# Performance work log

Measured on AMD Instinct MI355X. Metric: run time of the kernel, lower is better.

## Reference

```python
import jax, jax.numpy as jnp
import numpy as np

N, E, EE = 2048, 32768, 262144
CS, CZ, CG, NRBF = 384, 128, 16, 64
D_MIN, D_MAX = 0.0, 20.0
LN_EPS = 1e-5
EPS = 1e-8


def _p(key, shape, scale):
    return (jax.random.normal(key, shape, dtype=jnp.float32) * scale)


def setup_inputs() -> dict:
    key = jax.random.key(0)
    ks = jax.random.split(key, 40)
    inp = {
        "node_features": jax.random.normal(ks[0], (N, CS), dtype=jnp.float32),
        "node_trans": jax.random.normal(ks[1], (N, 3), dtype=jnp.float32) * 5.0,
        "dst_edge_features": jax.random.normal(ks[2], (E, CZ), dtype=jnp.float32),
        "dst_edge_index": jax.random.randint(ks[3], (2, E), 0, N),
        "src_edge_features": jax.random.normal(ks[4], (E, CZ), dtype=jnp.float32),
        "src_edge_index": jax.random.randint(ks[5], (2, E), 0, N),
        "edge_edge_index": jax.random.randint(ks[6], (2, EE), 0, E),
        # params (torch Linear math: y = x @ W + b, W stored [in,out])
        "w_nl": _p(ks[7], (CS, CG), 0.05), "b_nl": jnp.zeros((CG,), jnp.float32),
        "w_nr": _p(ks[8], (CS, CG), 0.05), "b_nr": jnp.zeros((CG,), jnp.float32),
        "g_dst": jnp.ones((CZ,), jnp.float32), "bt_dst": jnp.zeros((CZ,), jnp.float32),
        "g_src": jnp.ones((CZ,), jnp.float32), "bt_src": jnp.zeros((CZ,), jnp.float32),
        "w_ep": _p(ks[9], (CZ, CZ), 0.08), "b_ep": jnp.zeros((CZ,), jnp.float32),
        "w_eg": _p(ks[10], (CZ, CZ), 0.08), "b_eg": jnp.zeros((CZ,), jnp.float32),
        "w_dg": _p(ks[11], (CG * CG, CZ), 0.06), "b_dg": jnp.zeros((CZ,), jnp.float32),
        "w_dp": _p(ks[12], (NRBF, CZ), 0.1), "b_dp": jnp.zeros((CZ,), jnp.float32),
        "g_out": jnp.ones((CZ,), jnp.float32), "bt_out": jnp.zeros((CZ,), jnp.float32),
        "w_lo": _p(ks[13], (CZ, CZ), 0.08), "b_lo": jnp.zeros((CZ,), jnp.float32),
        "w_og": _p(ks[14], (CZ, CZ), 0.08), "b_og": jnp.zeros((CZ,), jnp.float32),
    }
    return inp


def _ln(x, g, b):
    m = jnp.mean(x, axis=-1, keepdims=True)
    v = jnp.mean(jnp.square(x - m), axis=-1, keepdims=True)
    return (x - m) * jax.lax.rsqrt(v + LN_EPS) * g + b


def _rbf(d):
    mu = jnp.linspace(D_MIN, D_MAX, NRBF)  # [NRBF]
    sigma = (D_MAX - D_MIN) / NRBF
    return jnp.exp(-jnp.square((d[:, None] - mu) / sigma))  # [EE, NRBF]


def reference(node_features, node_trans, dst_edge_features, dst_edge_index,
              src_edge_features, src_edge_index, edge_edge_index,
              w_nl, b_nl, w_nr, b_nr, g_dst, bt_dst, g_src, bt_src,
              w_ep, b_ep, w_eg, b_eg, w_dg, b_dg, w_dp, b_dp,
              g_out, bt_out, w_lo, b_lo, w_og, b_og):
    ee0 = edge_edge_index[0]  # index into dst edges
    ee1 = edge_edge_index[1]  # index into src edges
    n1 = src_edge_index[0][ee1]  # left node per edge-edge pair
    n2 = dst_edge_index[0][ee0]  # right node per edge-edge pair

    dst_ef = _ln(dst_edge_features, g_dst, bt_dst)
    src_ef = _ln(src_edge_features, g_src, bt_src)

    node_left = node_features @ w_nl + b_nl   # [N, CG]
    node_right = node_features @ w_nr + b_nr  # [N, CG]

    # per-pair outer product gate: [EE, CG*CG]
    edge3 = jnp.einsum('ei,ej->eij', node_left[n1], node_right[n2]).reshape(-1, CG * CG)
    edge3_gate = edge3 @ w_dg + b_dg  # [EE, CZ]

    diff = node_trans[n1] - node_trans[n2] + EPS
    dist = jnp.linalg.norm(diff, axis=-1)  # [EE]
    dist_feat = _rbf(dist) @ w_dp + b_dp   # [EE, CZ]
    edge3_features = jax.nn.sigmoid(edge3_gate) * dist_feat

    edge2 = jax.nn.sigmoid(src_ef @ w_eg + b_eg) * (src_ef @ w_ep + b_ep)  # [E, CZ]
    edge_update = edge2[ee0] * edge3_features  # [EE, CZ]
    edge_update = jax.ops.segment_sum(edge_update, ee0, num_segments=E)  # [E, CZ]

    edge_update = _ln(edge_update, g_out, bt_out)
    edge_update = edge_update @ w_lo + b_lo
    edge_update = edge_update * jax.nn.sigmoid(dst_ef @ w_og + b_og)
    return edge_update
```

## Files before the change

kernel.cpp:

```cpp
#include <hip/hip_runtime.h>
#include <hip/hip_bf16.h>
#include <math.h>

#define NN    2048
#define NE    32768
#define NP    262144
#define CS_   384
#define CZ_   128
#define CG_   16
#define NRBF_ 64

typedef __attribute__((ext_vector_type(8))) short bf16x8;
typedef __attribute__((ext_vector_type(4))) float f32x4;

__device__ __forceinline__ unsigned short f2bf(float f) {
  __hip_bfloat16 h = __float2bfloat16(f);
  union { __hip_bfloat16 h; unsigned short u; } cv; cv.h = h; return cv.u;
}

__global__ void k_nodeproj(const float* __restrict__ nf,
                           const float* __restrict__ wnl, const float* __restrict__ bnl,
                           const float* __restrict__ wnr, const float* __restrict__ bnr,
                           unsigned short* __restrict__ nl, unsigned short* __restrict__ nr) {
  const int n = blockIdx.x;
  const int t = threadIdx.x;
  if (t >= 32) return;
  const float* __restrict__ w = (t < 16) ? wnl : wnr;
  const int col = t & 15;
  const float* __restrict__ row = nf + (size_t)n * CS_;
  float acc = 0.f;
  #pragma unroll 8
  for (int k = 0; k < CS_; ++k) acc = fmaf(row[k], w[k * CG_ + col], acc);
  acc += (t < 16) ? bnl[col] : bnr[col];
  ((t < 16) ? nl : nr)[n * CG_ + col] = f2bf(acc);
}

__global__ void k_prepB(const float* __restrict__ wdg, const float* __restrict__ wdp,
                        unsigned short* __restrict__ frag) {
  const int idx = blockIdx.x * 256 + threadIdx.x;
  if (idx >= 40960) return;
  float v;
  if (idx < 32768) {
    const int e = idx & 7, l = (idx >> 3) & 63, ks = (idx >> 9) & 7, n = idx >> 12;
    const int k = ks * 32 + (l >> 4) * 8 + e, ch = n * 16 + (l & 15);
    v = wdg[(size_t)k * CZ_ + ch];
  } else {
    const int j = idx - 32768;
    const int e = j & 7, l = (j >> 3) & 63, ks2 = (j >> 9) & 1, n = j >> 10;
    const int k2 = ks2 * 32 + (l >> 4) * 8 + e, ch = n * 16 + (l & 15);
    v = wdp[(size_t)k2 * CZ_ + ch];
  }
  frag[idx] = f2bf(v);
}

__global__ void k_hist(const int* __restrict__ ee, int* __restrict__ hist) {
  const int p = blockIdx.x * 256 + threadIdx.x;
  atomicAdd(&hist[ee[p]], 1);
}

__global__ __launch_bounds__(1024) void k_scan(const int* __restrict__ hist,
                                               int* __restrict__ start) {
  __shared__ int tot[1024];
  const int t = threadIdx.x;
  const int base = t * 32;
  int s = 0;
  for (int k = 0; k < 32; ++k) s += hist[base + k];
  tot[t] = s;
  __syncthreads();
  for (int off = 1; off < 1024; off <<= 1) {
    int v = tot[t];
    int u = (t >= off) ? tot[t - off] : 0;
    __syncthreads();
    tot[t] = v + u;
    __syncthreads();
  }
  int run = (t == 0) ? 0 : tot[t - 1];
  for (int k = 0; k < 32; ++k) { start[base + k] = run; run += hist[base + k]; }
  if (t == 1023) start[32768] = run;
}

__global__ void k_scatter(const int* __restrict__ ee, const int* __restrict__ start,
                          int* __restrict__ cnt2, int* __restrict__ perm) {
  const int p = blockIdx.x * 256 + threadIdx.x;
  const int e = ee[p];
  const int idx = atomicAdd(&cnt2[e], 1);
  perm[start[e] + idx] = p;
}

__global__ __launch_bounds__(256) void k_edge2(
    const float* __restrict__ sef,
    const float* __restrict__ gs, const float* __restrict__ bs,
    const float* __restrict__ weg, const float* __restrict__ beg,
    const float* __restrict__ wep, const float* __restrict__ bep,
    float* __restrict__ edge2) {
  __shared__ float xln[32][132];
  const int tid = threadIdx.x;
  const int row0 = blockIdx.x * 32;
  {
    const int r = tid >> 3, s = tid & 7;
    const float* __restrict__ xp = sef + (size_t)(row0 + r) * CZ_ + s * 16;
    float v[16];
    #pragma unroll
    for (int q = 0; q < 4; ++q) {
      const float4 t4 = *(const float4*)(xp + 4 * q);
      v[4*q+0] = t4.x; v[4*q+1] = t4.y; v[4*q+2] = t4.z; v[4*q+3] = t4.w;
    }
    float sum = 0.f, sq = 0.f;
    #pragma unroll
    for (int q = 0; q < 16; ++q) { sum += v[q]; sq = fmaf(v[q], v[q], sq); }
    #pragma unroll
    for (int o = 1; o < 8; o <<= 1) { sum += __shfl_xor(sum, o); sq += __shfl_xor(sq, o); }
    const float mean = sum * (1.f / CZ_);
    const float rstd = rsqrtf(sq * (1.f / CZ_) - mean * mean + 1e-5f);
    const int kb = s * 16;
    #pragma unroll
    for (int q = 0; q < 16; ++q)
      xln[r][kb + q] = (v[q] - mean) * rstd * gs[kb + q] + bs[kb + q];
  }
  __syncthreads();

  const int c = tid & (CZ_ - 1);
  const int h = tid >> 7;
  float accg[16], accp[16];
  #pragma unroll
  for (int q = 0; q < 16; ++q) { accg[q] = 0.f; accp[q] = 0.f; }
  #pragma unroll 2
  for (int k = 0; k < CZ_; k += 4) {
    const float wg0 = weg[(size_t)(k+0)*CZ_ + c], wg1 = weg[(size_t)(k+1)*CZ_ + c],
                wg2 = weg[(size_t)(k+2)*CZ_ + c], wg3 = weg[(size_t)(k+3)*CZ_ + c];
    const float wp0 = wep[(size_t)(k+0)*CZ_ + c], wp1 = wep[(size_t)(k+1)*CZ_ + c],
                wp2 = wep[(size_t)(k+2)*CZ_ + c], wp3 = wep[(size_t)(k+3)*CZ_ + c];
    #pragma unroll
    for (int rr = 0; rr < 16; ++rr) {
      const float4 xv = *(const float4*)&xln[h*16 + rr][k];
      accg[rr] = fmaf(xv.x, wg0, accg[rr]); accg[rr] = fmaf(xv.y, wg1, accg[rr]);
      accg[rr] = fmaf(xv.z, wg2, accg[rr]); accg[rr] = fmaf(xv.w, wg3, accg[rr]);
      accp[rr] = fmaf(xv.x, wp0, accp[rr]); accp[rr] = fmaf(xv.y, wp1, accp[rr]);
      accp[rr] = fmaf(xv.z, wp2, accp[rr]); accp[rr] = fmaf(xv.w, wp3, accp[rr]);
    }
  }
  const float bg = beg[c], bp = bep[c];
  #pragma unroll
  for (int rr = 0; rr < 16; ++rr) {
    const float gate = 1.f / (1.f + __expf(-(accg[rr] + bg)));
    edge2[(size_t)(row0 + h*16 + rr) * CZ_ + c] = gate * (accp[rr] + bp);
  }
}

__global__ __launch_bounds__(256, 2) void k_pairfeat(
    const int* __restrict__ perm, const int* __restrict__ ee,
    const int* __restrict__ sei, const int* __restrict__ dei,
    const unsigned short* __restrict__ nlb, const unsigned short* __restrict__ nrb,
    const float* __restrict__ trans, const unsigned short* __restrict__ frag,
    const float* __restrict__ bdg, const float* __restrict__ bdp,
    unsigned int* __restrict__ feat) {
  __shared__ unsigned short sfrag[40960];
  const int tid = threadIdx.x;

  #pragma unroll
  for (int i = 0; i < 20; ++i)
    ((float4*)sfrag)[i * 256 + tid] = ((const float4*)frag)[i * 256 + tid];

  const int lane = tid & 63;
  const int w = tid >> 6;
  const int g = lane >> 4;
  const int c15 = lane & 15;
  const int rowbase = blockIdx.x * 128 + w * 32;

  unsigned int nlu[2][8], nru[2][8];
  float dist[2];
  #pragma unroll
  for (int m = 0; m < 2; ++m) {
    const int slot = rowbase + m * 16 + c15;
    const int p = perm[slot];
    const int e0 = ee[p];
    const int e1 = ee[NP + p];
    const int n1 = sei[e1];
    const int n2 = dei[e0];
    const uint4 a = ((const uint4*)(nlb + (size_t)n1 * CG_))[0];
    const uint4 b = ((const uint4*)(nlb + (size_t)n1 * CG_))[1];
    nlu[m][0]=a.x; nlu[m][1]=a.y; nlu[m][2]=a.z; nlu[m][3]=a.w;
    nlu[m][4]=b.x; nlu[m][5]=b.y; nlu[m][6]=b.z; nlu[m][7]=b.w;
    const uint4 c = ((const uint4*)(nrb + (size_t)n2 * CG_))[0];
    const uint4 d = ((const uint4*)(nrb + (size_t)n2 * CG_))[1];
    nru[m][0]=c.x; nru[m][1]=c.y; nru[m][2]=c.z; nru[m][3]=c.w;
    nru[m][4]=d.x; nru[m][5]=d.y; nru[m][6]=d.z; nru[m][7]=d.w;
    const float dx = trans[n1*3+0] - trans[n2*3+0] + 1e-8f;
    const float dy = trans[n1*3+1] - trans[n2*3+1] + 1e-8f;
    const float dz = trans[n1*3+2] - trans[n2*3+2] + 1e-8f;
    dist[m] = sqrtf(fmaf(dx, dx, fmaf(dy, dy, dz * dz)));
  }
  __syncthreads();

  f32x4 acc[2][8], acc2[2][8];
  #pragma unroll
  for (int m = 0; m < 2; ++m)
    #pragma unroll
    for (int n = 0; n < 8; ++n) { acc[m][n] = (f32x4)0.f; acc2[m][n] = (f32x4)0.f; }

  const bool hiI = (lane & 32) != 0;
  const bool hiJ = (lane & 16) != 0;

  #pragma unroll
  for (int ks = 0; ks < 8; ++ks) {
    bf16x8 af[2];
    #pragma unroll
    for (int m = 0; m < 2; ++m) {
      const unsigned wv = nlu[m][ks];
      const float nli = __uint_as_float(hiI ? (wv & 0xFFFF0000u) : (wv << 16));
      #pragma unroll
      for (int ep = 0; ep < 4; ++ep) {
        const unsigned wr = hiJ ? nru[m][4 + ep] : nru[m][ep];
        const float j0 = __uint_as_float(wr << 16);
        const float j1 = __uint_as_float(wr & 0xFFFF0000u);
        af[m][2*ep]   = (short)f2bf(nli * j0);
        af[m][2*ep+1] = (short)f2bf(nli * j1);
      }
    }
    #pragma unroll
    for (int n = 0; n < 8; ++n) {
      const bf16x8 bf = *(const bf16x8*)(sfrag + ((size_t)((n * 8 + ks) * 64 + lane)) * 8);
      acc[0][n] = __builtin_amdgcn_mfma_f32_16x16x32_bf16(af[0], bf, acc[0][n], 0, 0, 0);
      acc[1][n] = __builtin_amdgcn_mfma_f32_16x16x32_bf16(af[1], bf, acc[1][n], 0, 0, 0);
    }
  }

  const float MU_STEP = 20.f / 63.f;
  const float INV_SIG = 64.f / 20.f;
  #pragma unroll
  for (int ks2 = 0; ks2 < 2; ++ks2) {
    bf16x8 a2[2];
    const int k2b = ks2 * 32 + g * 8;
    #pragma unroll
    for (int m = 0; m < 2; ++m) {
      #pragma unroll
      for (int e = 0; e < 8; ++e) {
        const float mu = (float)(k2b + e) * MU_STEP;
        const float u = (dist[m] - mu) * INV_SIG;
        a2[m][e] = (short)f2bf(__expf(-u * u));
      }
    }
    #pragma unroll
    for (int n = 0; n < 8; ++n) {
      const bf16x8 b2 = *(const bf16x8*)(sfrag + 32768 + ((size_t)((n * 2 + ks2) * 64 + lane)) * 8);
      acc2[0][n] = __builtin_amdgcn_mfma_f32_16x16x32_bf16(a2[0], b2, acc2[0][n], 0, 0, 0);
      acc2[1][n] = __builtin_amdgcn_mfma_f32_16x16x32_bf16(a2[1], b2, acc2[1][n], 0, 0, 0);
    }
  }

  float bdgv[8], bdpv[8];
  #pragma unroll
  for (int n = 0; n < 8; ++n) { bdgv[n] = bdg[n*16 + c15]; bdpv[n] = bdp[n*16 + c15]; }

  #pragma unroll
  for (int m = 0; m < 2; ++m) {
    #pragma unroll
    for (int n = 0; n < 4; ++n) {
      #pragma unroll
      for (int r = 0; r < 4; ++r) {
        const float glo = __builtin_amdgcn_rcpf(1.f + __expf(-(acc[m][n][r] + bdgv[n])));
        const float ghi = __builtin_amdgcn_rcpf(1.f + __expf(-(acc[m][n+4][r] + bdgv[n+4])));
        const float lo = glo * (acc2[m][n][r] + bdpv[n]);
        const float hi = ghi * (acc2[m][n+4][r] + bdpv[n+4]);
        const unsigned u = (unsigned)f2bf(lo) | ((unsigned)f2bf(hi) << 16);
        const int row = rowbase + m * 16 + g * 4 + r;
        feat[(size_t)row * 64 + n * 16 + c15] = u;
      }
    }
  }
}

__global__ __launch_bounds__(64) void k_segsum(
    const int* __restrict__ start, const int* __restrict__ perm,
    const unsigned int* __restrict__ feat, float* __restrict__ e2) {
  __shared__ int lst[512];
  const int e = blockIdx.x;
  const int t = threadIdx.x;
  const int s0 = start[e], s1 = start[e + 1];
  const int deg = s1 - s0;
  float slo = 0.f, shi = 0.f;
  if (deg <= 512) {
    for (int i = t; i < deg; i += 64) lst[i] = (perm[s0 + i] << 9) | i;
    __syncthreads();
    if (t == 0) {
      for (int a = 1; a < deg; ++a) {
        const int v = lst[a];
        int b = a - 1;
        while (b >= 0 && lst[b] > v) { lst[b + 1] = lst[b]; --b; }
        lst[b + 1] = v;
      }
    }
    __syncthreads();
    for (int j = 0; j < deg; ++j) {
      const int slot = s0 + (lst[j] & 511);
      const unsigned u = feat[(size_t)slot * 64 + t];
      slo += __uint_as_float(u << 16);
      shi += __uint_as_float(u & 0xFFFF0000u);
    }
  } else {
    for (int j = 0; j < deg; ++j) {
      const unsigned u = feat[(size_t)(s0 + j) * 64 + t];
      slo += __uint_as_float(u << 16);
      shi += __uint_as_float(u & 0xFFFF0000u);
    }
  }
  const float p0 = e2[(size_t)e * CZ_ + t];
  const float p1 = e2[(size_t)e * CZ_ + 64 + t];
  e2[(size_t)e * CZ_ + t] = slo * p0;
  e2[(size_t)e * CZ_ + 64 + t] = shi * p1;
}

__global__ __launch_bounds__(256) void k_final(
    const float* __restrict__ prod, const float* __restrict__ def,
    const float* __restrict__ go, const float* __restrict__ bo,
    const float* __restrict__ gd, const float* __restrict__ bd,
    const float* __restrict__ wlo, const float* __restrict__ blo,
    const float* __restrict__ wog, const float* __restrict__ bog,
    float* __restrict__ out) {
  __shared__ float x1[32][132];
  __shared__ float x2[32][132];
  const int tid = threadIdx.x;
  const int row0 = blockIdx.x * 32;
  {
    const int r = tid >> 3, s = tid & 7;
    const int kb = s * 16;
    float v[16];
    {
      const float* __restrict__ ap = prod + (size_t)(row0 + r) * CZ_ + kb;
      #pragma unroll
      for (int q = 0; q < 4; ++q) {
        const float4 a4 = *(const float4*)(ap + 4*q);
        v[4*q+0]=a4.x; v[4*q+1]=a4.y; v[4*q+2]=a4.z; v[4*q+3]=a4.w;
      }
      float sum = 0.f, sq = 0.f;
      #pragma unroll
      for (int q = 0; q < 16; ++q) { sum += v[q]; sq = fmaf(v[q], v[q], sq); }
      #pragma unroll
      for (int o = 1; o < 8; o <<= 1) { sum += __shfl_xor(sum, o); sq += __shfl_xor(sq, o); }
      const float mean = sum * (1.f / CZ_);
      const float rstd = rsqrtf(sq * (1.f / CZ_) - mean * mean + 1e-5f);
      #pragma unroll
      for (int q = 0; q < 16; ++q)
        x1[r][kb+q] = (v[q] - mean) * rstd * go[kb+q] + bo[kb+q];
    }
    {
      const float* __restrict__ dp = def + (size_t)(row0 + r) * CZ_ + kb;
      #pragma unroll
      for (int q = 0; q < 4; ++q) {
        const float4 a4 = *(const float4*)(dp + 4*q);
        v[4*q+0]=a4.x; v[4*q+1]=a4.y; v[4*q+2]=a4.z; v[4*q+3]=a4.w;
      }
      float sum = 0.f, sq = 0.f;
      #pragma unroll
      for (int q = 0; q < 16; ++q) { sum += v[q]; sq = fmaf(v[q], v[q], sq); }
      #pragma unroll
      for (int o = 1; o < 8; o <<= 1) { sum += __shfl_xor(sum, o); sq += __shfl_xor(sq, o); }
      const float mean = sum * (1.f / CZ_);
      const float rstd = rsqrtf(sq * (1.f / CZ_) - mean * mean + 1e-5f);
      #pragma unroll
      for (int q = 0; q < 16; ++q)
        x2[r][kb+q] = (v[q] - mean) * rstd * gd[kb+q] + bd[kb+q];
    }
  }
  __syncthreads();

  const int c = tid & (CZ_ - 1);
  const int h = tid >> 7;
  float accy[16], accg[16];
  #pragma unroll
  for (int q = 0; q < 16; ++q) { accy[q] = 0.f; accg[q] = 0.f; }
  #pragma unroll 2
  for (int k = 0; k < CZ_; k += 4) {
    const float wl0 = wlo[(size_t)(k+0)*CZ_ + c], wl1 = wlo[(size_t)(k+1)*CZ_ + c],
                wl2 = wlo[(size_t)(k+2)*CZ_ + c], wl3 = wlo[(size_t)(k+3)*CZ_ + c];
    const float wo0 = wog[(size_t)(k+0)*CZ_ + c], wo1 = wog[(size_t)(k+1)*CZ_ + c],
                wo2 = wog[(size_t)(k+2)*CZ_ + c], wo3 = wog[(size_t)(k+3)*CZ_ + c];
    #pragma unroll
    for (int rr = 0; rr < 16; ++rr) {
      const float4 xv1 = *(const float4*)&x1[h*16 + rr][k];
      const float4 xv2 = *(const float4*)&x2[h*16 + rr][k];
      accy[rr] = fmaf(xv1.x, wl0, accy[rr]); accy[rr] = fmaf(xv1.y, wl1, accy[rr]);
      accy[rr] = fmaf(xv1.z, wl2, accy[rr]); accy[rr] = fmaf(xv1.w, wl3, accy[rr]);
      accg[rr] = fmaf(xv2.x, wo0, accg[rr]); accg[rr] = fmaf(xv2.y, wo1, accg[rr]);
      accg[rr] = fmaf(xv2.z, wo2, accg[rr]); accg[rr] = fmaf(xv2.w, wo3, accg[rr]);
    }
  }
  const float bl = blo[c], bgv = bog[c];
  #pragma unroll
  for (int rr = 0; rr < 16; ++rr) {
    const float y = accy[rr] + bl;
    const float gsig = 1.f / (1.f + __expf(-(accg[rr] + bgv)));
    out[(size_t)(row0 + h*16 + rr) * CZ_ + c] = y * gsig;
  }
}

extern "C" void kernel_launch(void* const* d_in, const int* in_sizes, int n_in,
                              void* d_out, int out_size, void* d_ws, size_t ws_size,
                              hipStream_t stream) {
  const float* nf     = (const float*)d_in[0];
  const float* trans  = (const float*)d_in[1];
  const float* dst_ef = (const float*)d_in[2];
  const int*   dst_ei = (const int*)d_in[3];
  const float* src_ef = (const float*)d_in[4];
  const int*   src_ei = (const int*)d_in[5];
  const int*   ee     = (const int*)d_in[6];
  const float* w_nl  = (const float*)d_in[7];  const float* b_nl  = (const float*)d_in[8];
  const float* w_nr  = (const float*)d_in[9];  const float* b_nr  = (const float*)d_in[10];
  const float* g_dst = (const float*)d_in[11]; const float* bt_dst= (const float*)d_in[12];
  const float* g_src = (const float*)d_in[13]; const float* bt_src= (const float*)d_in[14];
  const float* w_ep  = (const float*)d_in[15]; const float* b_ep  = (const float*)d_in[16];
  const float* w_eg  = (const float*)d_in[17]; const float* b_eg  = (const float*)d_in[18];
  const float* w_dg  = (const float*)d_in[19]; const float* b_dg  = (const float*)d_in[20];
  const float* w_dp  = (const float*)d_in[21]; const float* b_dp  = (const float*)d_in[22];
  const float* g_out = (const float*)d_in[23]; const float* bt_out= (const float*)d_in[24];
  const float* w_lo  = (const float*)d_in[25]; const float* b_lo  = (const float*)d_in[26];
  const float* w_og  = (const float*)d_in[27]; const float* b_og  = (const float*)d_in[28];

  char* ws = (char*)d_ws;
  size_t off = 0;
  unsigned int* feat = (unsigned int*)(ws + off); off += (size_t)NP * 64 * 4;
  float*        e2   = (float*)(ws + off);        off += (size_t)NE * CZ_ * 4;
  unsigned short* nlb = (unsigned short*)(ws + off); off += (size_t)NN * CG_ * 2;
  unsigned short* nrb = (unsigned short*)(ws + off); off += (size_t)NN * CG_ * 2;
  unsigned short* frag = (unsigned short*)(ws + off); off += 81920;
  int* hist  = (int*)(ws + off); off += 32768 * 4;
  int* start = (int*)(ws + off); off += 32772 * 4;
  int* cnt2  = (int*)(ws + off); off += 32768 * 4;
  int* perm  = (int*)(ws + off); off += (size_t)NP * 4;

  hipMemsetAsync(hist, 0, (char*)perm - (char*)hist, stream);

  k_nodeproj<<<NN, 64, 0, stream>>>(nf, w_nl, b_nl, w_nr, b_nr, nlb, nrb);
  k_prepB<<<160, 256, 0, stream>>>(w_dg, w_dp, frag);
  k_hist<<<NP / 256, 256, 0, stream>>>(ee, hist);
  k_scan<<<1, 1024, 0, stream>>>(hist, start);
  k_scatter<<<NP / 256, 256, 0, stream>>>(ee, start, cnt2, perm);
  k_edge2<<<NE / 32, 256, 0, stream>>>(src_ef, g_src, bt_src, w_eg, b_eg, w_ep, b_ep, e2);
  k_pairfeat<<<NP / 128, 256, 0, stream>>>(perm, ee, src_ei, dst_ei, nlb, nrb, trans,
                                           frag, b_dg, b_dp, feat);
  k_segsum<<<NE, 64, 0, stream>>>(start, perm, feat, e2);
  k_final<<<NE / 32, 256, 0, stream>>>(e2, dst_ef, g_out, bt_out, g_dst, bt_dst,
                                       w_lo, b_lo, w_og, b_og, (float*)d_out);
}
```

Measured before the change: 231.2 us.

## Use split-bf16 MFMA for dense GEMMs and split pair features into two fp32 passes

Replaces the scalar FMA GEMMs in edge2 and final with MFMA kernels that use a hi/lo bf16 split (three MFMAs per tile) to keep near-fp32 accuracy. The RBF projection also gets the hi/lo split. Pair features are now written in unpermuted order as fp32 and split into two channel halves, each followed by its own segment-sum pass that sorts and gathers by perm. The change also reuses hist as the scatter cursor to drop one memset region, and writes into the output buffer directly. The cost is extra MFMA work, double the feature write traffic per channel, two extra kernel launches, and scattered gathers in segsum.

Result: slower. 244.0 us (+5.5%).

```diff
diff --git a/kernel.cpp b/kernel.cpp
--- a/kernel.cpp
+++ b/kernel.cpp
@@ -16,6 +16,12 @@
 __device__ __forceinline__ unsigned short f2bf(float f) {
   __hip_bfloat16 h = __float2bfloat16(f);
   union { __hip_bfloat16 h; unsigned short u; } cv; cv.h = h; return cv.u;
+}
+__device__ __forceinline__ float bfbits(unsigned short h) {
+  return __uint_as_float((unsigned)h << 16);
+}
+__device__ __forceinline__ float sigf(float x) {
+  return __builtin_amdgcn_rcpf(1.f + __expf(-x));
 }
 
 __global__ void k_nodeproj(const float* __restrict__ nf,
@@ -35,22 +41,36 @@
   ((t < 16) ? nl : nr)[n * CG_ + col] = f2bf(acc);
 }
 
-__global__ void k_prepB(const float* __restrict__ wdg, const float* __restrict__ wdp,
-                        unsigned short* __restrict__ frag) {
+__global__ void k_prep(const float* __restrict__ wdg, const float* __restrict__ wdp,
+                       const float* __restrict__ weg, const float* __restrict__ wep,
+                       const float* __restrict__ wlo, const float* __restrict__ wog,
+                       unsigned short* __restrict__ frag) {
   const int idx = blockIdx.x * 256 + threadIdx.x;
-  if (idx >= 40960) return;
-  float v;
+  if (idx >= 180224) return;
   if (idx < 32768) {
     const int e = idx & 7, l = (idx >> 3) & 63, ks = (idx >> 9) & 7, n = idx >> 12;
-    const int k = ks * 32 + (l >> 4) * 8 + e, ch = n * 16 + (l & 15);
-    v = wdg[(size_t)k * CZ_ + ch];
-  } else {
+    frag[idx] = f2bf(wdg[(size_t)(ks * 32 + (l >> 4) * 8 + e) * CZ_ + n * 16 + (l & 15)]);
+  } else if (idx < 40960) {
     const int j = idx - 32768;
     const int e = j & 7, l = (j >> 3) & 63, ks2 = (j >> 9) & 1, n = j >> 10;
-    const int k2 = ks2 * 32 + (l >> 4) * 8 + e, ch = n * 16 + (l & 15);
-    v = wdp[(size_t)k2 * CZ_ + ch];
-  }
-  frag[idx] = f2bf(v);
+    frag[idx] = f2bf(wdp[(size_t)(ks2 * 32 + (l >> 4) * 8 + e) * CZ_ + n * 16 + (l & 15)]);
+  } else if (idx < 172032) {
+    const bool lo = idx >= 106496;
+    const int j2 = (idx - 40960) & 65535;
+    const int m = j2 >> 14;
+    const float* __restrict__ mp = (m == 0) ? weg : (m == 1) ? wep : (m == 2) ? wlo : wog;
+    const int j = j2 & 16383;
+    const int e = j & 7, l = (j >> 3) & 63, ks = (j >> 9) & 3, n = j >> 11;
+    const float v = mp[(size_t)(ks * 32 + (l >> 4) * 8 + e) * CZ_ + n * 16 + (l & 15)];
+    const unsigned short h = f2bf(v);
+    frag[idx] = lo ? f2bf(v - bfbits(h)) : h;
+  } else {
+    const int j = idx - 172032;
+    const int e = j & 7, l = (j >> 3) & 63, ks2 = (j >> 9) & 1, n = j >> 10;
+    const float v = wdp[(size_t)(ks2 * 32 + (l >> 4) * 8 + e) * CZ_ + n * 16 + (l & 15)];
+    const unsigned short h = f2bf(v);
+    frag[idx] = f2bf(v - bfbits(h));
+  }
 }
 
 __global__ void k_hist(const int* __restrict__ ee, int* __restrict__ hist) {
@@ -58,7 +78,7 @@
   atomicAdd(&hist[ee[p]], 1);
 }
 
-__global__ __launch_bounds__(1024) void k_scan(const int* __restrict__ hist,
+__global__ __launch_bounds__(1024) void k_scan(int* __restrict__ hist,
                                                int* __restrict__ start) {
   __shared__ int tot[1024];
   const int t = threadIdx.x;
@@ -75,91 +95,135 @@
     __syncthreads();
   }
   int run = (t == 0) ? 0 : tot[t - 1];
-  for (int k = 0; k < 32; ++k) { start[base + k] = run; run += hist[base + k]; }
+  for (int k = 0; k < 32; ++k) {
+    const int h = hist[base + k];
+    start[base + k] = run;
+    run += h;
+    hist[base + k] = 0;
+  }
   if (t == 1023) start[32768] = run;
 }
 
 __global__ void k_scatter(const int* __restrict__ ee, const int* __restrict__ start,
-                          int* __restrict__ cnt2, int* __restrict__ perm) {
+                          int* __restrict__ cursor, int* __restrict__ perm) {
   const int p = blockIdx.x * 256 + threadIdx.x;
   const int e = ee[p];
-  const int idx = atomicAdd(&cnt2[e], 1);
+  const int idx = atomicAdd(&cursor[e], 1);
   perm[start[e] + idx] = p;
 }
 
-__global__ __launch_bounds__(256) void k_edge2(
+__device__ __forceinline__ void ln_to_frag2(
+    const float* __restrict__ src, const float* __restrict__ gam,
+    const float* __restrict__ bet, int row0, int tid,
+    unsigned short (* __restrict__ afh)[64][8],
+    unsigned short (* __restrict__ afl)[64][8]) {
+  const int r = tid >> 2, qt = tid & 3;
+  const float* __restrict__ xp = src + (size_t)(row0 + r) * CZ_ + qt * 32;
+  float v[32];
+  #pragma unroll
+  for (int j = 0; j < 8; ++j) {
+    const float4 t4 = ((const float4*)xp)[j];
+    v[4*j+0] = t4.x; v[4*j+1] = t4.y; v[4*j+2] = t4.z; v[4*j+3] = t4.w;
+  }
+  float sum = 0.f, sq = 0.f;
+  #pragma unroll
+  for (int q = 0; q < 32; ++q) { sum += v[q]; sq = fmaf(v[q], v[q], sq); }
+  sum += __shfl_xor(sum, 1); sq += __shfl_xor(sq, 1);
+  sum += __shfl_xor(sum, 2); sq += __shfl_xor(sq, 2);
+  const float mean = sum * (1.f / CZ_);
+  const float rstd = rsqrtf(sq * (1.f / CZ_) - mean * mean + 1e-5f);
+  const int fb = (r >> 4) * 4 + qt;
+  const int r15 = r & 15;
+  #pragma unroll
+  for (int g = 0; g < 4; ++g) {
+    unsigned pkh[4], pkl[4];
+    #pragma unroll
+    for (int h2 = 0; h2 < 4; ++h2) {
+      const int c0 = qt * 32 + g * 8 + 2 * h2;
+      const float f0 = (v[g*8+2*h2]   - mean) * rstd * gam[c0]   + bet[c0];
+      const float f1 = (v[g*8+2*h2+1] - mean) * rstd * gam[c0+1] + bet[c0+1];
+      const unsigned short h0 = f2bf(f0), h1 = f2bf(f1);
+      const unsigned short l0 = f2bf(f0 - bfbits(h0)), l1 = f2bf(f1 - bfbits(h1));
+      pkh[h2] = (unsigned)h0 | ((unsigned)h1 << 16);
+      pkl[h2] = (unsigned)l0 | ((unsigned)l1 << 16);
+    }
+    *(uint4*)&afh[fb][g * 16 + r15][0] = make_uint4(pkh[0], pkh[1], pkh[2], pkh[3]);
+    *(uint4*)&afl[fb][g * 16 + r15][0] = make_uint4(pkl[0], pkl[1], pkl[2], pkl[3]);
+  }
+}
+
+__global__ __launch_bounds__(256) void k_edge2_mfma(
     const float* __restrict__ sef,
     const float* __restrict__ gs, const float* __restrict__ bs,
-    const float* __restrict__ weg, const float* __restrict__ beg,
-    const float* __restrict__ wep, const float* __restrict__ bep,
-    float* __restrict__ edge2) {
-  __shared__ float xln[32][132];
+    const unsigned short* __restrict__ wf,
+    const float* __restrict__ beg, const float* __restrict__ bep,
+    float* __restrict__ e2) {
+  __shared__ unsigned short afh[16][64][8];
+  __shared__ unsigned short afl[16][64][8];
   const int tid = threadIdx.x;
-  const int row0 = blockIdx.x * 32;
-  {
-    const int r = tid >> 3, s = tid & 7;
-    const float* __restrict__ xp = sef + (size_t)(row0 + r) * CZ_ + s * 16;
-    float v[16];
-    #pragma unroll
-    for (int q = 0; q < 4; ++q) {
-      const float4 t4 = *(const float4*)(xp + 4 * q);
-      v[4*q+0] = t4.x; v[4*q+1] = t4.y; v[4*q+2] = t4.z; v[4*q+3] = t4.w;
-    }
-    float sum = 0.f, sq = 0.f;
-    #pragma unroll
-    for (int q = 0; q < 16; ++q) { sum += v[q]; sq = fmaf(v[q], v[q], sq); }
-    #pragma unroll
-    for (int o = 1; o < 8; o <<= 1) { sum += __shfl_xor(sum, o); sq += __shfl_xor(sq, o); }
-    const float mean = sum * (1.f / CZ_);
-    const float rstd = rsqrtf(sq * (1.f / CZ_) - mean * mean + 1e-5f);
-    const int kb = s * 16;
-    #pragma unroll
-    for (int q = 0; q < 16; ++q)
-      xln[r][kb + q] = (v[q] - mean) * rstd * gs[kb + q] + bs[kb + q];
-  }
+  const int row0 = blockIdx.x * 64;
+  ln_to_frag2(sef, gs, bs, row0, tid, afh, afl);
   __syncthreads();
 
-  const int c = tid & (CZ_ - 1);
-  const int h = tid >> 7;
-  float accg[16], accp[16];
-  #pragma unroll
-  for (int q = 0; q < 16; ++q) { accg[q] = 0.f; accp[q] = 0.f; }
-  #pragma unroll 2
-  for (int k = 0; k < CZ_; k += 4) {
-    const float wg0 = weg[(size_t)(k+0)*CZ_ + c], wg1 = weg[(size_t)(k+1)*CZ_ + c],
-                wg2 = weg[(size_t)(k+2)*CZ_ + c], wg3 = weg[(size_t)(k+3)*CZ_ + c];
-    const float wp0 = wep[(size_t)(k+0)*CZ_ + c], wp1 = wep[(size_t)(k+1)*CZ_ + c],
-                wp2 = wep[(size_t)(k+2)*CZ_ + c], wp3 = wep[(size_t)(k+3)*CZ_ + c];
-    #pragma unroll
-    for (int rr = 0; rr < 16; ++rr) {
-      const float4 xv = *(const float4*)&xln[h*16 + rr][k];
-      accg[rr] = fmaf(xv.x, wg0, accg[rr]); accg[rr] = fmaf(xv.y, wg1, accg[rr]);
-      accg[rr] = fmaf(xv.z, wg2, accg[rr]); accg[rr] = fmaf(xv.w, wg3, accg[rr]);
-      accp[rr] = fmaf(xv.x, wp0, accp[rr]); accp[rr] = fmaf(xv.y, wp1, accp[rr]);
-      accp[rr] = fmaf(xv.z, wp2, accp[rr]); accp[rr] = fmaf(xv.w, wp3, accp[rr]);
-    }
-  }
-  const float bg = beg[c], bp = bep[c];
-  #pragma unroll
-  for (int rr = 0; rr < 16; ++rr) {
-    const float gate = 1.f / (1.f + __expf(-(accg[rr] + bg)));
-    edge2[(size_t)(row0 + h*16 + rr) * CZ_ + c] = gate * (accp[rr] + bp);
-  }
-}
-
+  const int lane = tid & 63;
+  const int w = tid >> 6;
+  f32x4 c1[8], c2[8];
+  #pragma unroll
+  for (int n = 0; n < 8; ++n) { c1[n] = (f32x4)0.f; c2[n] = (f32x4)0.f; }
+  #pragma unroll
+  for (int ks = 0; ks < 4; ++ks) {
+    const bf16x8 ah = *(const bf16x8*)&afh[w * 4 + ks][lane][0];
+    const bf16x8 al = *(const bf16x8*)&afl[w * 4 + ks][lane][0];
+    #pragma unroll
+    for (int n = 0; n < 8; ++n) {
+      const size_t bo = ((size_t)((n * 4 + ks) * 64 + lane)) * 8;
+      const bf16x8 b1h = *(const bf16x8*)(wf + bo);
+      const bf16x8 b1l = *(const bf16x8*)(wf + 65536 + bo);
+      const bf16x8 b2h = *(const bf16x8*)(wf + 16384 + bo);
+      const bf16x8 b2l = *(const bf16x8*)(wf + 81920 + bo);
+      c1[n] = __builtin_amdgcn_mfma_f32_16x16x32_bf16(ah, b1h, c1[n], 0, 0, 0);
+      c1[n] = __builtin_amdgcn_mfma_f32_16x16x32_bf16(al, b1h, c1[n], 0, 0, 0);
+      c1[n] = __builtin_amdgcn_mfma_f32_16x16x32_bf16(ah, b1l, c1[n], 0, 0, 0);
+      c2[n] = __builtin_amdgcn_mfma_f32_16x16x32_bf16(ah, b2h, c2[n], 0, 0, 0);
+      c2[n] = __builtin_amdgcn_mfma_f32_16x16x32_bf16(al, b2h, c2[n], 0, 0, 0);
+      c2[n] = __builtin_amdgcn_mfma_f32_16x16x32_bf16(ah, b2l, c2[n], 0, 0, 0);
+    }
+  }
+  const int c15 = lane & 15, rq = lane >> 4;
+  #pragma unroll
+  for (int n = 0; n < 8; ++n) {
+    const int ch = n * 16 + c15;
+    const float bg = beg[ch], bp = bep[ch];
+    #pragma unroll
+    for (int r = 0; r < 4; ++r) {
+      const int row = row0 + w * 16 + rq * 4 + r;
+      e2[(size_t)row * CZ_ + ch] = sigf(c1[n][r] + bg) * (c2[n][r] + bp);
+    }
+  }
+}
+
+template <int CC>
 __global__ __launch_bounds__(256, 2) void k_pairfeat(
-    const int* __restrict__ perm, const int* __restrict__ ee,
+    const int* __restrict__ ee,
     const int* __restrict__ sei, const int* __restrict__ dei,
     const unsigned short* __restrict__ nlb, const unsigned short* __restrict__ nrb,
     const float* __restrict__ trans, const unsigned short* __restrict__ frag,
     const float* __restrict__ bdg, const float* __restrict__ bdp,
-    unsigned int* __restrict__ feat) {
-  __shared__ unsigned short sfrag[40960];
+    float* __restrict__ feat) {
+  __shared__ unsigned short sfrag[20480];
   const int tid = threadIdx.x;
 
-  #pragma unroll
-  for (int i = 0; i < 20; ++i)
-    ((float4*)sfrag)[i * 256 + tid] = ((const float4*)frag)[i * 256 + tid];
+  {
+    const unsigned short* __restrict__ gsrc = frag + CC * 16384;
+    #pragma unroll
+    for (int i = 0; i < 8; ++i)
+      ((float4*)sfrag)[i * 256 + tid] = ((const float4*)gsrc)[i * 256 + tid];
+    const unsigned short* __restrict__ rsrc = frag + 32768 + CC * 4096;
+    #pragma unroll
+    for (int i = 0; i < 2; ++i)
+      ((float4*)(sfrag + 16384))[i * 256 + tid] = ((const float4*)rsrc)[i * 256 + tid];
+  }
+  const unsigned short* __restrict__ wf2l = frag + 172032 + CC * 4096;
 
   const int lane = tid & 63;
   const int w = tid >> 6;
@@ -171,8 +235,7 @@
   float dist[2];
   #pragma unroll
   for (int m = 0; m < 2; ++m) {
-    const int slot = rowbase + m * 16 + c15;
-    const int p = perm[slot];
+    const int p = rowbase + m * 16 + c15;
     const int e0 = ee[p];
     const int e1 = ee[NP + p];
     const int n1 = sei[e1];
@@ -192,11 +255,11 @@
   }
   __syncthreads();
 
-  f32x4 acc[2][8], acc2[2][8];
+  f32x4 acc[2][4], acc2[2][4];
   #pragma unroll
   for (int m = 0; m < 2; ++m)
     #pragma unroll
-    for (int n = 0; n < 8; ++n) { acc[m][n] = (f32x4)0.f; acc2[m][n] = (f32x4)0.f; }
+    for (int n = 0; n < 4; ++n) { acc[m][n] = (f32x4)0.f; acc2[m][n] = (f32x4)0.f; }
 
   const bool hiI = (lane & 32) != 0;
   const bool hiJ = (lane & 16) != 0;
@@ -218,7 +281,7 @@
       }
     }
     #pragma unroll
-    for (int n = 0; n < 8; ++n) {
+    for (int n = 0; n < 4; ++n) {
       const bf16x8 bf = *(const bf16x8*)(sfrag + ((size_t)((n * 8 + ks) * 64 + lane)) * 8);
       acc[0][n] = __builtin_amdgcn_mfma_f32_16x16x32_bf16(af[0], bf, acc[0][n], 0, 0, 0);
       acc[1][n] = __builtin_amdgcn_mfma_f32_16x16x32_bf16(af[1], bf, acc[1][n], 0, 0, 0);
@@ -229,7 +292,7 @@
   const float INV_SIG = 64.f / 20.f;
   #pragma unroll
   for (int ks2 = 0; ks2 < 2; ++ks2) {
-    bf16x8 a2[2];
+    bf16x8 a2h[2], a2l[2];
     const int k2b = ks2 * 32 + g * 8;
     #pragma unroll
     for (int m = 0; m < 2; ++m) {
@@ -237,20 +300,32 @@
       for (int e = 0; e < 8; ++e) {
         const float mu = (float)(k2b + e) * MU_STEP;
         const float u = (dist[m] - mu) * INV_SIG;
-        a2[m][e] = (short)f2bf(__expf(-u * u));
+        const float ev = __expf(-u * u);
+        const unsigned short h = f2bf(ev);
+        a2h[m][e] = (short)h;
+        a2l[m][e] = (short)f2bf(ev - bfbits(h));
       }
     }
     #pragma unroll
-    for (int n = 0; n < 8; ++n) {
-      const bf16x8 b2 = *(const bf16x8*)(sfrag + 32768 + ((size_t)((n * 2 + ks2) * 64 + lane)) * 8);
-      acc2[0][n] = __builtin_amdgcn_mfma_f32_16x16x32_bf16(a2[0], b2, acc2[0][n], 0, 0, 0);
-      acc2[1][n] = __builtin_amdgcn_mfma_f32_16x16x32_bf16(a2[1], b2, acc2[1][n], 0, 0, 0);
-    }
-  }
-
-  float bdgv[8], bdpv[8];
-  #pragma unroll
-  for (int n = 0; n < 8; ++n) { bdgv[n] = bdg[n*16 + c15]; bdpv[n] = bdp[n*16 + c15]; }
+    for (int n = 0; n < 4; ++n) {
+      const size_t bo = ((size_t)((n * 2 + ks2) * 64 + lane)) * 8;
+      const bf16x8 b2h = *(const bf16x8*)(sfrag + 16384 + bo);
+      const bf16x8 b2l = *(const bf16x8*)(wf2l + bo);
+      acc2[0][n] = __builtin_amdgcn_mfma_f32_16x16x32_bf16(a2h[0], b2h, acc2[0][n], 0, 0, 0);
+      acc2[0][n] = __builtin_amdgcn_mfma_f32_16x16x32_bf16(a2l[0], b2h, acc2[0][n], 0, 0, 0);
+      acc2[0][n] = __builtin_amdgcn_mfma_f32_16x16x32_bf16(a2h[0], b2l, acc2[0][n], 0, 0, 0);
+      acc2[1][n] = __builtin_amdgcn_mfma_f32_16x16x32_bf16(a2h[1], b2h, acc2[1][n], 0, 0, 0);
+      acc2[1][n] = __builtin_amdgcn_mfma_f32_16x16x32_bf16(a2l[1], b2h, acc2[1][n], 0, 0, 0);
+      acc2[1][n] = __builtin_amdgcn_mfma_f32_16x16x32_bf16(a2h[1], b2l, acc2[1][n], 0, 0, 0);
+    }
+  }
+
+  float bdgv[4], bdpv[4];
+  #pragma unroll
+  for (int n = 0; n < 4; ++n) {
+    bdgv[n] = bdg[(CC * 4 + n) * 16 + c15];
+    bdpv[n] = bdp[(CC * 4 + n) * 16 + c15];
+  }
 
   #pragma unroll
   for (int m = 0; m < 2; ++m) {
@@ -258,13 +333,9 @@
     for (int n = 0; n < 4; ++n) {
       #pragma unroll
       for (int r = 0; r < 4; ++r) {
-        const float glo = __builtin_amdgcn_rcpf(1.f + __expf(-(acc[m][n][r] + bdgv[n])));
-        const float ghi = __builtin_amdgcn_rcpf(1.f + __expf(-(acc[m][n+4][r] + bdgv[n+4])));
-        const float lo = glo * (acc2[m][n][r] + bdpv[n]);
-        const float hi = ghi * (acc2[m][n+4][r] + bdpv[n+4]);
-        const unsigned u = (unsigned)f2bf(lo) | ((unsigned)f2bf(hi) << 16);
+        const float gv = sigf(acc[m][n][r] + bdgv[n]);
         const int row = rowbase + m * 16 + g * 4 + r;
-        feat[(size_t)row * 64 + n * 16 + c15] = u;
+        feat[(size_t)row * 64 + n * 16 + c15] = gv * (acc2[m][n][r] + bdpv[n]);
       }
     }
   }
@@ -272,15 +343,15 @@
 
 __global__ __launch_bounds__(64) void k_segsum(
     const int* __restrict__ start, const int* __restrict__ perm,
-    const unsigned int* __restrict__ feat, float* __restrict__ e2) {
+    const float* __restrict__ feat, float* __restrict__ e2, int cc) {
   __shared__ int lst[512];
   const int e = blockIdx.x;
   const int t = threadIdx.x;
   const int s0 = start[e], s1 = start[e + 1];
   const int deg = s1 - s0;
-  float slo = 0.f, shi = 0.f;
+  float s = 0.f;
   if (deg <= 512) {
-    for (int i = t; i < deg; i += 64) lst[i] = (perm[s0 + i] << 9) | i;
+    for (int i = t; i < deg; i += 64) lst[i] = perm[s0 + i];
     __syncthreads();
     if (t == 0) {
       for (int a = 1; a < deg; ++a) {
@@ -291,106 +362,76 @@
       }
     }
     __syncthreads();
+    for (int j = 0; j < deg; ++j)
+      s += feat[(size_t)lst[j] * 64 + t];
+  } else {
+    int last = -1;
     for (int j = 0; j < deg; ++j) {
-      const int slot = s0 + (lst[j] & 511);
-      const unsigned u = feat[(size_t)slot * 64 + t];
-      slo += __uint_as_float(u << 16);
-      shi += __uint_as_float(u & 0xFFFF0000u);
-    }
-  } else {
-    for (int j = 0; j < deg; ++j) {
-      const unsigned u = feat[(size_t)(s0 + j) * 64 + t];
-      slo += __uint_as_float(u << 16);
-      shi += __uint_as_float(u & 0xFFFF0000u);
-    }
-  }
-  const float p0 = e2[(size_t)e * CZ_ + t];
-  const float p1 = e2[(size_t)e * CZ_ + 64 + t];
-  e2[(size_t)e * CZ_ + t] = slo * p0;
-  e2[(size_t)e * CZ_ + 64 + t] = shi * p1;
-}
-
-__global__ __launch_bounds__(256) void k_final(
-    const float* __restrict__ prod, const float* __restrict__ def,
+      int mn = 0x7fffffff;
+      for (int i = 0; i < deg; ++i) {
+        const int p = perm[s0 + i];
+        if (p > last && p < mn) mn = p;
+      }
+      last = mn;
+      s += feat[(size_t)mn * 64 + t];
+    }
+  }
+  float* __restrict__ dst = e2 + (size_t)e * CZ_ + cc * 64 + t;
+  *dst = s * (*dst);
+}
+
+__global__ __launch_bounds__(256) void k_final_mfma(
+    float* po, const float* __restrict__ def,
     const float* __restrict__ go, const float* __restrict__ bo,
     const float* __restrict__ gd, const float* __restrict__ bd,
-    const float* __restrict__ wlo, const float* __restrict__ blo,
-    const float* __restrict__ wog, const float* __restrict__ bog,
-    float* __restrict__ out) {
-  __shared__ float x1[32][132];
-  __shared__ float x2[32][132];
+    const unsigned short* __restrict__ wf,
+    const float* __restrict__ blo, const float* __restrict__ bog) {
+  __shared__ unsigned short af1h[16][64][8];
+  __shared__ unsigned short af1l[16][64][8];
+  __shared__ unsigned short af2h[16][64][8];
+  __shared__ unsigned short af2l[16][64][8];
   const int tid = threadIdx.x;
-  const int row0 = blockIdx.x * 32;
-  {
-    const int r = tid >> 3, s = tid & 7;
-    const int kb = s * 16;
-    float v[16];
-    {
-      const float* __restrict__ ap = prod + (size_t)(row0 + r) * CZ_ + kb;
-      #pragma unroll
-      for (int q = 0; q < 4; ++q) {
-        const float4 a4 = *(const float4*)(ap + 4*q);
-        v[4*q+0]=a4.x; v[4*q+1]=a4.y; v[4*q+2]=a4.z; v[4*q+3]=a4.w;
-      }
-      float sum = 0.f, sq = 0.f;
-      #pragma unroll
-      for (int q = 0; q < 16; ++q) { sum += v[q]; sq = fmaf(v[q], v[q], sq); }
-      #pragma unroll
-      for (int o = 1; o < 8; o <<= 1) { sum += __shfl_xor(sum, o); sq += __shfl_xor(sq, o); }
-      const float mean = sum * (1.f / CZ_);
-      const float rstd = rsqrtf(sq * (1.f / CZ_) - mean * mean + 1e-5f);
-      #pragma unroll
-      for (int q = 0; q < 16; ++q)
-        x1[r][kb+q] = (v[q] - mean) * rstd * go[kb+q] + bo[kb+q];
-    }
-    {
-      const float* __restrict__ dp = def + (size_t)(row0 + r) * CZ_ + kb;
-      #pragma unroll
-      for (int q = 0; q < 4; ++q) {
-        const float4 a4 = *(const float4*)(dp + 4*q);
-        v[4*q+0]=a4.x; v[4*q+1]=a4.y; v[4*q+2]=a4.z; v[4*q+3]=a4.w;
-      }
-      float sum = 0.f, sq = 0.f;
-      #pragma unroll
-      for (int q = 0; q < 16; ++q) { sum += v[q]; sq = fmaf(v[q], v[q], sq); }
-      #pragma unroll
-      for (int o = 1; o < 8; o <<= 1) { sum += __shfl_xor(sum, o); sq += __shfl_xor(sq, o); }
-      const float mean = sum * (1.f / CZ_);
-      const float rstd = rsqrtf(sq * (1.f / CZ_) - mean * mean + 1e-5f);
-      #pragma unroll
-      for (int q = 0; q < 16; ++q)
-        x2[r][kb+q] = (v[q] - mean) * rstd * gd[kb+q] + bd[kb+q];
-    }
-  }
+  const int row0 = blockIdx.x * 64;
+  ln_to_frag2(po, go, bo, row0, tid, af1h, af1l);
+  ln_to_frag2(def, gd, bd, row0, tid, af2h, af2l);
   __syncthreads();
 
-  const int c = tid & (CZ_ - 1);
-  const int h = tid >> 7;
-  float accy[16], accg[16];
-  #pragma unroll
-  for (int q = 0; q < 16; ++q) { accy[q] = 0.f; accg[q] = 0.f; }
-  #pragma unroll 2
-  for (int k = 0; k < CZ_; k += 4) {
-    const float wl0 = wlo[(size_t)(k+0)*CZ_ + c], wl1 = wlo[(size_t)(k+1)*CZ_ + c],
-                wl2 = wlo[(size_t)(k+2)*CZ_ + c], wl3 = wlo[(size_t)(k+3)*CZ_ + c];
-    const float wo0 = wog[(size_t)(k+0)*CZ_ + c], wo1 = wog[(size_t)(k+1)*CZ_ + c],
-                wo2 = wog[(size_t)(k+2)*CZ_ + c], wo3 = wog[(size_t)(k+3)*CZ_ + c];
-    #pragma unroll
-    for (int rr = 0; rr < 16; ++rr) {
-      const float4 xv1 = *(const float4*)&x1[h*16 + rr][k];
-      const float4 xv2 = *(const float4*)&x2[h*16 + rr][k];
-      accy[rr] = fmaf(xv1.x, wl0, accy[rr]); accy[rr] = fmaf(xv1.y, wl1, accy[rr]);
-      accy[rr] = fmaf(xv1.z, wl2, accy[rr]); accy[rr] = fmaf(xv1.w, wl3, accy[rr]);
-      accg[rr] = fmaf(xv2.x, wo0, accg[rr]); accg[rr] = fmaf(xv2.y, wo1, accg[rr]);
-      accg[rr] = fmaf(xv2.z, wo2, accg[rr]); accg[rr] = fmaf(xv2.w, wo3, accg[rr]);
-    }
-  }
-  const float bl = blo[c], bgv = bog[c];
-  #pragma unroll
-  for (int rr = 0; rr < 16; ++rr) {
-    const float y = accy[rr] + bl;
-    const float gsig = 1.f / (1.f + __expf(-(accg[rr] + bgv)));
-    out[(size_t)(row0 + h*16 + rr) * CZ_ + c] = y * gsig;
+  const int lane = tid & 63;
+  const int w = tid >> 6;
+  f32x4 c1[8], c2[8];
+  #pragma unroll
+  for (int n = 0; n < 8; ++n) { c1[n] = (f32x4)0.f; c2[n] = (f32x4)0.f; }
+  #pragma unroll
+  for (int ks = 0; ks < 4; ++ks) {
+    const bf16x8 a1h = *(const bf16x8*)&af1h[w * 4 + ks][lane][0];
+    const bf16x8 a1l = *(const bf16x8*)&af1l[w * 4 + ks][lane][0];
+    const bf16x8 a2h = *(const bf16x8*)&af2h[w * 4 + ks][lane][0];
+    const bf16x8 a2l = *(const bf16x8*)&af2l[w * 4 + ks][lane][0];
+    #pragma unroll
+    for (int n = 0; n < 8; ++n) {
+      const size_t bo = ((size_t)((n * 4 + ks) * 64 + lane)) * 8;
+      const bf16x8 b1h = *(const bf16x8*)(wf + bo);
+      const bf16x8 b1l = *(const bf16x8*)(wf + 65536 + bo);
+      const bf16x8 b2h = *(const bf16x8*)(wf + 16384 + bo);
+      const bf16x8 b2l = *(const bf16x8*)(wf + 81920 + bo);
+      c1[n] = __builtin_amdgcn_mfma_f32_16x16x32_bf16(a1h, b1h, c1[n], 0, 0, 0);
+      c1[n] = __builtin_amdgcn_mfma_f32_16x16x32_bf16(a1l, b1h, c1[n], 0, 0, 0);
+      c1[n] = __builtin_amdgcn_mfma_f32_16x16x32_bf16(a1h, b1l, c1[n], 0, 0, 0);
+      c2[n] = __builtin_amdgcn_mfma_f32_16x16x32_bf16(a2h, b2h, c2[n], 0, 0, 0);
+      c2[n] = __builtin_amdgcn_mfma_f32_16x16x32_bf16(a2l, b2h, c2[n], 0, 0, 0);
+      c2[n] = __builtin_amdgcn_mfma_f32_16x16x32_bf16(a2h, b2l, c2[n], 0, 0, 0);
+    }
+  }
+  const int c15 = lane & 15, rq = lane >> 4;
+  #pragma unroll
+  for (int n = 0; n < 8; ++n) {
+    const int ch = n * 16 + c15;
+    const float bl = blo[ch], bg = bog[ch];
+    #pragma unroll
+    for (int r = 0; r < 4; ++r) {
+      const int row = row0 + w * 16 + rq * 4 + r;
+      po[(size_t)row * CZ_ + ch] = (c1[n][r] + bl) * sigf(c2[n][r] + bg);
+    }
   }
 }
 
@@ -416,29 +457,37 @@
   const float* w_lo  = (const float*)d_in[25]; const float* b_lo  = (const float*)d_in[26];
   const float* w_og  = (const float*)d_in[27]; const float* b_og  = (const float*)d_in[28];
 
+  float* e2 = (float*)d_out;
+
   char* ws = (char*)d_ws;
   size_t off = 0;
-  unsigned int* feat = (unsigned int*)(ws + off); off += (size_t)NP * 64 * 4;
-  float*        e2   = (float*)(ws + off);        off += (size_t)NE * CZ_ * 4;
+  float*        feat = (float*)(ws + off);        off += (size_t)NP * 64 * 4;
   unsigned short* nlb = (unsigned short*)(ws + off); off += (size_t)NN * CG_ * 2;
   unsigned short* nrb = (unsigned short*)(ws + off); off += (size_t)NN * CG_ * 2;
-  unsigned short* frag = (unsigned short*)(ws + off); off += 81920;
+  unsigned short* frag = (unsigned short*)(ws + off); off += 180224 * 2;
   int* hist  = (int*)(ws + off); off += 32768 * 4;
   int* start = (int*)(ws + off); off += 32772 * 4;
-  int* cnt2  = (int*)(ws + off); off += 32768 * 4;
   int* perm  = (int*)(ws + off); off += (size_t)NP * 4;
 
-  hipMemsetAsync(hist, 0, (char*)perm - (char*)hist, stream);
+  const unsigned short* wf_pair = frag;
+  const unsigned short* wf_e2   = frag + 40960;
+  const unsigned short* wf_fin  = frag + 40960 + 32768;
+
+  hipMemsetAsync(hist, 0, 32768 * 4, stream);
 
   k_nodeproj<<<NN, 64, 0, stream>>>(nf, w_nl, b_nl, w_nr, b_nr, nlb, nrb);
-  k_prepB<<<160, 256, 0, stream>>>(w_dg, w_dp, frag);
+  k_prep<<<704, 256, 0, stream>>>(w_dg, w_dp, w_eg, w_ep, w_lo, w_og,
+                                  (unsigned short*)frag);
   k_hist<<<NP / 256, 256, 0, stream>>>(ee, hist);
   k_scan<<<1, 1024, 0, stream>>>(hist, start);
-  k_scatter<<<NP / 256, 256, 0, stream>>>(ee, start, cnt2, perm);
-  k_edge2<<<NE / 32, 256, 0, stream>>>(src_ef, g_src, bt_src, w_eg, b_eg, w_ep, b_ep, e2);
-  k_pairfeat<<<NP / 128, 256, 0, stream>>>(perm, ee, src_ei, dst_ei, nlb, nrb, trans,
-                                           frag, b_dg, b_dp, feat);
-  k_segsum<<<NE, 64, 0, stream>>>(start, perm, feat, e2);
-  k_final<<<NE / 32, 256, 0, stream>>>(e2, dst_ef, g_out, bt_out, g_dst, bt_dst,
-                                       w_lo, b_lo, w_og, b_og, (float*)d_out);
-}
+  k_scatter<<<NP / 256, 256, 0, stream>>>(ee, start, hist, perm);
+  k_edge2_mfma<<<NE / 64, 256, 0, stream>>>(src_ef, g_src, bt_src, wf_e2, b_eg, b_ep, e2);
+  k_pairfeat<0><<<NP / 128, 256, 0, stream>>>(ee, src_ei, dst_ei, nlb, nrb, trans,
+                                              wf_pair, b_dg, b_dp, feat);
+  k_segsum<<<NE, 64, 0, stream>>>(start, perm, feat, e2, 0);
+  k_pairfeat<1><<<NP / 128, 256, 0, stream>>>(ee, src_ei, dst_ei, nlb, nrb, trans,
+                                              wf_pair, b_dg, b_dp, feat);
+  k_segsum<<<NE, 64, 0, stream>>>(start, perm, feat, e2, 1);
+  k_final_mfma<<<NE / 64, 256, 0, stream>>>(e2, dst_ef, g_out, bt_out, g_dst, bt_dst,
+                                            wf_fin, b_lo, b_og);
+}
```
